# Kernel tuning notes

Hardware: AMD Instinct MI355X
Metric: run time of the kernel (lower is better)

Reference implementation:

```python
import jax, jax.numpy as jnp
import numpy as np
from jax import lax

HID, PROJ, DYN = 256, 256, 64
HW, BS, NQ = 6400, 16, 100


def setup_inputs() -> dict:
    key = jax.random.key(0)
    ks = jax.random.split(key, 10)
    p = lambda k, shape: jax.random.normal(k, shape, jnp.float32) * 0.02
    return {
        "query_feat": jax.random.normal(ks[0], (HW, BS, HID), jnp.float32),
        "support_feat": jax.random.normal(ks[1], (NQ, BS, HID), jnp.float32),
        "h": 80,
        "w": 80,
        "Wq": p(ks[2], (HID, PROJ)), "bq": jnp.zeros((PROJ,), jnp.float32),
        "Ws": p(ks[3], (HID, PROJ)), "bsp": jnp.zeros((PROJ,), jnp.float32),
        "W1": p(ks[4], (PROJ, DYN)), "b1": jnp.zeros((DYN,), jnp.float32),
        "W2": p(ks[5], (DYN, HID)), "b2": jnp.zeros((HID,), jnp.float32),
    }


def reference(query_feat, support_feat, h, w, Wq, bq, Ws, bsp, W1, b1, W2, b2):
    # query_feat: [hw, bs, c] -> [bs, hw, c]; support_feat: [nq, bs, c] -> [bs, nq, c]
    qf = jnp.transpose(query_feat, (1, 0, 2))
    sf = jnp.transpose(support_feat, (1, 0, 2))
    bsz, nq = sf.shape[0], sf.shape[1]
    hw = h * w

    fs_proj = sf @ Ws + bsp                      # [bs, nq, proj]
    fq_proj = qf @ Wq + bq                       # [bs, hw, proj]
    pattern = jnp.tanh(jax.nn.relu(fs_proj @ W1 + b1) @ W2 + b2)
    fs_feat = (pattern + 1.0) * fs_proj          # [bs, nq, proj]

    # bmm(fq, fs^T).T -> [bs, nq, hw]
    sim = jnp.einsum("bkp,bnp->bnk", fq_proj, fs_feat)
    similarity = sim.reshape(bsz, nq, h, w)

    # coordinate grid: x varies along w, y along h; flattened [hw, 2]
    gy = jnp.arange(h, dtype=jnp.float32) + 0.5
    gx = jnp.arange(w, dtype=jnp.float32) + 0.5
    X, Y = jnp.meshgrid(gx, gy, indexing="xy")  # each [h, w]
    coord = jnp.stack([X, Y], axis=-1).reshape(hw, 2)
    side = jnp.array([w, h], dtype=jnp.float32)

    sm = jax.nn.softmax(sim, axis=-1)            # [bs, nq, hw]
    proposal_for_loss = jnp.einsum("bnk,kd->bnd", sm, coord) / side

    # argmax peak -> one-hot -> 3x3 max-pool dilation (note (w,h) reshape per original)
    max_pos = jnp.argmax(sim, axis=-1)           # [bs, nq]
    max_mask = jax.nn.one_hot(max_pos, hw, dtype=jnp.float32).reshape(bsz, nq, w, h)
    local_mask = lax.reduce_window(
        max_mask, -jnp.inf, lax.max,
        window_dimensions=(1, 1, 3, 3), window_strides=(1, 1, 1, 1),
        padding=[(0, 0), (0, 0), (1, 1), (1, 1)],
    ).reshape(bsz, nq, hw)

    local_sm = sm * local_mask
    local_sm = local_sm / (jnp.sum(local_sm, axis=-1, keepdims=True) + 1e-10)
    proposals = jnp.einsum("bnk,kd->bnd", local_sm, coord) / side

    return proposal_for_loss, similarity, proposals
```

## Files before the change

### kernel.cpp

```cpp
#include <hip/hip_runtime.h>

#define HID 256
#define PROJ 256
#define DYN 64
#define HWD 6400
#define BSZ 16
#define NQ 100
#define HH 80
#define WW 80

typedef unsigned short u16;
typedef u16 u16x8 __attribute__((ext_vector_type(8)));
typedef __bf16 bf16x8 __attribute__((ext_vector_type(8)));
typedef float f32x4 __attribute__((ext_vector_type(4)));

__device__ __forceinline__ float bf2f(u16 h) {
    union { unsigned u; float f; } c; c.u = ((unsigned)h) << 16; return c.f;
}
__device__ __forceinline__ u16 f2bf(float f) {
    union { float f; unsigned u; } c; c.f = f;
    return (u16)((c.u + 0x7FFFu + ((c.u >> 16) & 1u)) >> 16);
}

__global__ __launch_bounds__(1024, 1) void kpre(
    const float* __restrict__ support,
    const float* __restrict__ Wq, const float* __restrict__ bq,
    const float* __restrict__ Ws, const float* __restrict__ bsp,
    const float* __restrict__ W1, const float* __restrict__ b1,
    const float* __restrict__ W2, const float* __restrict__ b2,
    u16* __restrict__ pack, float* __restrict__ cvec)
{
    const int c = blockIdx.x;
    const int b = blockIdx.y;
    const int t = threadIdx.x;

    __shared__ __align__(16) float sf_t[HID][8];
    __shared__ __align__(16) float part[4][8][256];
    __shared__ __align__(16) float fsp[8][PROJ];
    __shared__ __align__(16) float hidp[2][8][DYN];
    __shared__ __align__(16) float hid[8][DYN];
    __shared__ __align__(16) float fsf_t[PROJ][8];
    __shared__ float cacc[8][4];

    const int g = t >> 8;
    const int p = t & 255;

    {
        const int nl = t >> 7;
        const int i0 = (t & 127) * 2;
        const int n = c * 8 + nl;
        float v0 = 0.f, v1 = 0.f;
        if (n < NQ) {
            const float* sp = support + (size_t)n * (BSZ * HID) + (size_t)b * HID + i0;
            const float2 a = *reinterpret_cast<const float2*>(sp);
            v0 = a.x; v1 = a.y;
        }
        sf_t[i0][nl] = v0;
        sf_t[i0 + 1][nl] = v1;
    }
    __syncthreads();

    {
        float acc[8];
        #pragma unroll
        for (int n = 0; n < 8; ++n) acc[n] = 0.f;
        const int ibase = g * 64;
        #pragma unroll
        for (int ib = 0; ib < 64; ib += 32) {
            float w[32];
            #pragma unroll
            for (int j = 0; j < 32; ++j)
                w[j] = Ws[(size_t)(ibase + ib + j) * PROJ + p];
            #pragma unroll
            for (int j = 0; j < 32; ++j) {
                const f32x4 s0 = *reinterpret_cast<const f32x4*>(&sf_t[ibase + ib + j][0]);
                const f32x4 s1 = *reinterpret_cast<const f32x4*>(&sf_t[ibase + ib + j][4]);
                acc[0] += s0[0] * w[j]; acc[1] += s0[1] * w[j];
                acc[2] += s0[2] * w[j]; acc[3] += s0[3] * w[j];
                acc[4] += s1[0] * w[j]; acc[5] += s1[1] * w[j];
                acc[6] += s1[2] * w[j]; acc[7] += s1[3] * w[j];
            }
        }
        #pragma unroll
        for (int n = 0; n < 8; ++n) part[g][n][p] = acc[n];
    }
    __syncthreads();
    {
        const int na = t >> 8;
        const float bb = bsp[p];
        #pragma unroll
        for (int k = 0; k < 2; ++k) {
            const int n = na + k * 4;
            fsp[n][p] = part[0][n][p] + part[1][n][p] + part[2][n][p] + part[3][n][p] + bb;
        }
    }
    __syncthreads();

    {
        const int ph = t >> 9;
        const int n = (t >> 6) & 7;
        const int d = t & 63;
        float a = 0.f;
        const int pb0 = ph * 128;
        #pragma unroll
        for (int pb = 0; pb < 128; pb += 32) {
            float w[32];
            #pragma unroll
            for (int j = 0; j < 32; ++j)
                w[j] = W1[(size_t)(pb0 + pb + j) * DYN + d];
            #pragma unroll
            for (int j = 0; j < 32; j += 4) {
                const f32x4 s = *reinterpret_cast<const f32x4*>(&fsp[n][pb0 + pb + j]);
                a += s[0] * w[j] + s[1] * w[j + 1] + s[2] * w[j + 2] + s[3] * w[j + 3];
            }
        }
        hidp[ph][n][d] = a;
    }
    __syncthreads();
    if (t < 512) {
        const int n = t >> 6, d = t & 63;
        const float a = hidp[0][n][d] + hidp[1][n][d] + b1[d];
        hid[n][d] = a > 0.f ? a : 0.f;
    }
    __syncthreads();

    {
        const int nh = t >> 8;
        const int n0 = nh * 2, n1 = nh * 2 + 1;
        const float bqv = bq[p];
        const float b2v = b2[p];
        float w[64];
        #pragma unroll
        for (int d = 0; d < 64; ++d) w[d] = W2[(size_t)d * PROJ + p];
        float a0 = 0.f, a1 = 0.f;
        #pragma unroll
        for (int d0 = 0; d0 < 64; d0 += 4) {
            const f32x4 h0 = *reinterpret_cast<const f32x4*>(&hid[n0][d0]);
            const f32x4 h1 = *reinterpret_cast<const f32x4*>(&hid[n1][d0]);
            a0 += h0[0] * w[d0] + h0[1] * w[d0 + 1] + h0[2] * w[d0 + 2] + h0[3] * w[d0 + 3];
            a1 += h1[0] * w[d0] + h1[1] * w[d0 + 1] + h1[2] * w[d0 + 2] + h1[3] * w[d0 + 3];
        }
        const float pat0 = tanhf(a0 + b2v);
        const float pat1 = tanhf(a1 + b2v);
        const float ff0 = (pat0 + 1.f) * fsp[n0][p];
        const float ff1 = (pat1 + 1.f) * fsp[n1][p];
        *reinterpret_cast<float2*>(&fsf_t[p][n0]) = make_float2(ff0, ff1);
        float cp0 = bqv * ff0, cp1 = bqv * ff1;
        for (int off = 32; off > 0; off >>= 1) {
            cp0 += __shfl_down(cp0, off);
            cp1 += __shfl_down(cp1, off);
        }
        const int lane = t & 63;
        const int ps = (t >> 6) & 3;
        if (lane == 0) { cacc[n0][ps] = cp0; cacc[n1][ps] = cp1; }
    }
    __syncthreads();
    if (t < 8) {
        const int n = c * 8 + t;
        if (n < NQ) cvec[b * NQ + n] = cacc[t][0] + cacc[t][1] + cacc[t][2] + cacc[t][3];
    }

    {
        const int h = p;
        float acc[8];
        #pragma unroll
        for (int n = 0; n < 8; ++n) acc[n] = 0.f;
        const int pbase = g * 64;
        #pragma unroll
        for (int pb = 0; pb < 64; pb += 32) {
            f32x4 wv4[8];
            #pragma unroll
            for (int k = 0; k < 8; ++k)
                wv4[k] = *reinterpret_cast<const f32x4*>(Wq + (size_t)h * PROJ + pbase + pb + k * 4);
            #pragma unroll
            for (int k = 0; k < 8; ++k) {
                #pragma unroll
                for (int m = 0; m < 4; ++m) {
                    const int pp = pbase + pb + k * 4 + m;
                    const float w = wv4[k][m];
                    const f32x4 f0 = *reinterpret_cast<const f32x4*>(&fsf_t[pp][0]);
                    const f32x4 f1 = *reinterpret_cast<const f32x4*>(&fsf_t[pp][4]);
                    acc[0] += f0[0] * w; acc[1] += f0[1] * w;
                    acc[2] += f0[2] * w; acc[3] += f0[3] * w;
                    acc[4] += f1[0] * w; acc[5] += f1[1] * w;
                    acc[6] += f1[2] * w; acc[7] += f1[3] * w;
                }
            }
        }
        #pragma unroll
        for (int n = 0; n < 8; ++n) part[g][n][h] = acc[n];
    }
    __syncthreads();

    {
        const int h = p;
        const int na = t >> 8;
        const int ks = h >> 5, quad = (h >> 3) & 3, j = h & 7;
        const int nt = c >> 1;
        #pragma unroll
        for (int k = 0; k < 2; ++k) {
            const int nl = na + k * 4;
            const int n = c * 8 + nl;
            float f = part[0][nl][h] + part[1][nl][h] + part[2][nl][h] + part[3][nl][h];
            if (n >= NQ) f = 0.f;
            const u16 hi = f2bf(f);
            const u16 lo = f2bf(f - bf2f(hi));
            const int nit = (c & 1) * 8 + nl;
            const int lane2 = quad * 16 + nit;
            const size_t base = ((((size_t)b * 2 + 0) * 8 + ks) * 8 + nt) * 512 + lane2 * 8 + j;
            pack[base] = hi;
            pack[base + (size_t)8 * 8 * 512] = lo;
        }
    }
}

__global__ __launch_bounds__(256, 4) void ksim(
    const float* __restrict__ qf,
    const u16* __restrict__ pack,
    const float* __restrict__ cvec,
    float* __restrict__ sim)
{
    const int mc = blockIdx.x;
    const int b  = blockIdx.y;
    const int wv = threadIdx.x >> 6;
    const int lane = threadIdx.x & 63;
    const int quad = lane >> 4, l16 = lane & 15;

    f32x4 acc[7];
    #pragma unroll
    for (int nt = 0; nt < 7; ++nt) acc[nt] = (f32x4){0.f, 0.f, 0.f, 0.f};

    const int row = mc * 64 + wv * 16 + l16;
    const float* ap = qf + (size_t)row * (BSZ * HID) + b * HID + quad * 8;
    const u16* pb = pack + (size_t)b * (2 * 8 * 8 * 64 * 8) + (size_t)lane * 8;

    f32x4 a0 = *reinterpret_cast<const f32x4*>(ap + 0);
    f32x4 a1 = *reinterpret_cast<const f32x4*>(ap + 4);

    #pragma unroll
    for (int ks = 0; ks < 8; ++ks) {
        u16x8 uh[7], ul[7];
        #pragma unroll
        for (int nt = 0; nt < 7; ++nt) {
            uh[nt] = *reinterpret_cast<const u16x8*>(pb + ((size_t)(0 * 8 + ks) * 8 + nt) * 512);
            ul[nt] = *reinterpret_cast<const u16x8*>(pb + ((size_t)(1 * 8 + ks) * 8 + nt) * 512);
        }
        f32x4 n0, n1;
        if (ks < 7) {
            n0 = *reinterpret_cast<const f32x4*>(ap + (ks + 1) * 32 + 0);
            n1 = *reinterpret_cast<const f32x4*>(ap + (ks + 1) * 32 + 4);
        }
        bf16x8 ahi, alo;
        #pragma unroll
        for (int j = 0; j < 4; ++j) {
            const float v = a0[j];
            const __bf16 h = (__bf16)v;
            ahi[j] = h; alo[j] = (__bf16)(v - (float)h);
        }
        #pragma unroll
        for (int j = 0; j < 4; ++j) {
            const float v = a1[j];
            const __bf16 h = (__bf16)v;
            ahi[4 + j] = h; alo[4 + j] = (__bf16)(v - (float)h);
        }
        #pragma unroll
        for (int nt = 0; nt < 7; ++nt) {
            const bf16x8 bh = __builtin_bit_cast(bf16x8, uh[nt]);
            const bf16x8 bl = __builtin_bit_cast(bf16x8, ul[nt]);
            acc[nt] = __builtin_amdgcn_mfma_f32_16x16x32_bf16(ahi, bh, acc[nt], 0, 0, 0);
            acc[nt] = __builtin_amdgcn_mfma_f32_16x16x32_bf16(ahi, bl, acc[nt], 0, 0, 0);
            acc[nt] = __builtin_amdgcn_mfma_f32_16x16x32_bf16(alo, bh, acc[nt], 0, 0, 0);
        }
        a0 = n0; a1 = n1;
    }

    const int kbase = mc * 64 + wv * 16 + quad * 4;
    #pragma unroll
    for (int nt = 0; nt < 7; ++nt) {
        const int n = nt * 16 + l16;
        if (n >= NQ) continue;
        const float cadd = cvec[b * NQ + n];
        f32x4 o = acc[nt];
        o[0] += cadd; o[1] += cadd; o[2] += cadd; o[3] += cadd;
        *reinterpret_cast<f32x4*>(sim + (size_t)(b * NQ + n) * HWD + kbase) = o;
    }
}

__global__ __launch_bounds__(64, 4) void kfin(
    const float* __restrict__ sim,
    float* __restrict__ out)
{
    const int bn = blockIdx.x;
    const int lane = threadIdx.x;
    const float* src = sim + (size_t)bn * HWD;

    f32x4 v[25];
    #pragma unroll
    for (int j = 0; j < 25; ++j)
        v[j] = *reinterpret_cast<const f32x4*>(src + j * 256 + lane * 4);

    float bv = -3.4e38f; int bi = 0;
    #pragma unroll
    for (int j = 0; j < 25; ++j) {
        #pragma unroll
        for (int k = 0; k < 4; ++k) {
            if (v[j][k] > bv) { bv = v[j][k]; bi = j * 256 + lane * 4 + k; }
        }
    }
    #pragma unroll
    for (int m = 1; m < 64; m <<= 1) {
        const float ov = __shfl_xor(bv, m);
        const int oi = __shfl_xor(bi, m);
        if (ov > bv || (ov == bv && oi < bi)) { bv = ov; bi = oi; }
    }
    const int xc = bi % WW, yc = bi / WW;

    float s1 = 0.f, sx = 0.f, sy = 0.f;
    float wl = 0.f, wx = 0.f, wyv = 0.f;
    int x = (lane * 4) % WW, y = (lane * 4) / WW;
    #pragma unroll
    for (int j = 0; j < 25; ++j) {
        #pragma unroll
        for (int k = 0; k < 4; ++k) {
            int xe = x + k, ye = y;
            if (xe >= WW) { xe -= WW; ye += 1; }
            const float e = __expf(v[j][k] - bv);
            const float fx = (float)xe + 0.5f;
            const float fy = (float)ye + 0.5f;
            s1 += e; sx += e * fx; sy += e * fy;
            const int dx = xe - xc, dy = ye - yc;
            const bool inw = (dx >= -1 && dx <= 1 && dy >= -1 && dy <= 1);
            const float ew = inw ? e : 0.f;
            wl += ew; wx += ew * fx; wyv += ew * fy;
        }
        x += 16; y += 3;
        if (x >= WW) { x -= WW; y += 1; }
    }
    #pragma unroll
    for (int m = 1; m < 64; m <<= 1) {
        s1 += __shfl_xor(s1, m);
        sx += __shfl_xor(sx, m);
        sy += __shfl_xor(sy, m);
        wl += __shfl_xor(wl, m);
        wx += __shfl_xor(wx, m);
        wyv += __shfl_xor(wyv, m);
    }

    if (lane == 0) {
        const float invS = 1.f / s1;
        out[(size_t)bn * 2 + 0] = sx * invS / (float)WW;
        out[(size_t)bn * 2 + 1] = sy * invS / (float)HH;
        const float den = wl + 1e-10f * s1;
        const size_t pbase = 3200 + (size_t)BSZ * NQ * HWD;
        out[pbase + (size_t)bn * 2 + 0] = wx / den / (float)WW;
        out[pbase + (size_t)bn * 2 + 1] = wyv / den / (float)HH;
    }
}

extern "C" void kernel_launch(void* const* d_in, const int* in_sizes, int n_in,
                              void* d_out, int out_size, void* d_ws, size_t ws_size,
                              hipStream_t stream) {
    const float* qf  = (const float*)d_in[0];
    const float* sf  = (const float*)d_in[1];
    const float* Wq  = (const float*)d_in[4];
    const float* bq  = (const float*)d_in[5];
    const float* Ws  = (const float*)d_in[6];
    const float* bsp = (const float*)d_in[7];
    const float* W1  = (const float*)d_in[8];
    const float* b1  = (const float*)d_in[9];
    const float* W2  = (const float*)d_in[10];
    const float* b2  = (const float*)d_in[11];

    u16*   pack  = (u16*)d_ws;
    float* cvec  = (float*)((char*)d_ws + 2097152);
    float* out   = (float*)d_out;
    float* sim   = out + 3200;

    kpre<<<dim3(14, 16), 1024, 0, stream>>>(sf, Wq, bq, Ws, bsp, W1, b1, W2, b2, pack, cvec);
    ksim<<<dim3(100, 16), 256, 0, stream>>>(qf, pack, cvec, sim);
    kfin<<<1600, 64, 0, stream>>>(sim, out);
}
```

Measured before the change: 271.6 us.

## Split kfin rows across two waves and batch weight loads with sched barriers

The final softmax/argmax kernel now uses two waves per row, each handling about half of the 6400 elements. Partial argmax and weighted sums are combined through shared memory. In kpre, weight loads are batched into larger register arrays, and sched_barrier keeps all loads issued before the FMAs, which raises memory-level parallelism; ksim gets a similar barrier. This costs more registers and an extra block-level sync in kfin.

```diff
diff --git a/kernel.cpp b/kernel.cpp
--- a/kernel.cpp
+++ b/kernel.cpp
@@ -65,21 +65,19 @@
         #pragma unroll
         for (int n = 0; n < 8; ++n) acc[n] = 0.f;
         const int ibase = g * 64;
-        #pragma unroll
-        for (int ib = 0; ib < 64; ib += 32) {
-            float w[32];
-            #pragma unroll
-            for (int j = 0; j < 32; ++j)
-                w[j] = Ws[(size_t)(ibase + ib + j) * PROJ + p];
-            #pragma unroll
-            for (int j = 0; j < 32; ++j) {
-                const f32x4 s0 = *reinterpret_cast<const f32x4*>(&sf_t[ibase + ib + j][0]);
-                const f32x4 s1 = *reinterpret_cast<const f32x4*>(&sf_t[ibase + ib + j][4]);
-                acc[0] += s0[0] * w[j]; acc[1] += s0[1] * w[j];
-                acc[2] += s0[2] * w[j]; acc[3] += s0[3] * w[j];
-                acc[4] += s1[0] * w[j]; acc[5] += s1[1] * w[j];
-                acc[6] += s1[2] * w[j]; acc[7] += s1[3] * w[j];
-            }
+        float w[64];
+        #pragma unroll
+        for (int j = 0; j < 64; ++j)
+            w[j] = Ws[(size_t)(ibase + j) * PROJ + p];
+        __builtin_amdgcn_sched_barrier(0);
+        #pragma unroll
+        for (int j = 0; j < 64; ++j) {
+            const f32x4 s0 = *reinterpret_cast<const f32x4*>(&sf_t[ibase + j][0]);
+            const f32x4 s1 = *reinterpret_cast<const f32x4*>(&sf_t[ibase + j][4]);
+            acc[0] += s0[0] * w[j]; acc[1] += s0[1] * w[j];
+            acc[2] += s0[2] * w[j]; acc[3] += s0[3] * w[j];
+            acc[4] += s1[0] * w[j]; acc[5] += s1[1] * w[j];
+            acc[6] += s1[2] * w[j]; acc[7] += s1[3] * w[j];
         }
         #pragma unroll
         for (int n = 0; n < 8; ++n) part[g][n][p] = acc[n];
@@ -103,13 +101,14 @@
         float a = 0.f;
         const int pb0 = ph * 128;
         #pragma unroll
-        for (int pb = 0; pb < 128; pb += 32) {
-            float w[32];
+        for (int pb = 0; pb < 128; pb += 64) {
+            float w[64];
             #pragma unroll
-            for (int j = 0; j < 32; ++j)
+            for (int j = 0; j < 64; ++j)
                 w[j] = W1[(size_t)(pb0 + pb + j) * DYN + d];
+            __builtin_amdgcn_sched_barrier(0);
             #pragma unroll
-            for (int j = 0; j < 32; j += 4) {
+            for (int j = 0; j < 64; j += 4) {
                 const f32x4 s = *reinterpret_cast<const f32x4*>(&fsp[n][pb0 + pb + j]);
                 a += s[0] * w[j] + s[1] * w[j + 1] + s[2] * w[j + 2] + s[3] * w[j + 3];
             }
@@ -132,6 +131,7 @@
         float w[64];
         #pragma unroll
         for (int d = 0; d < 64; ++d) w[d] = W2[(size_t)d * PROJ + p];
+        __builtin_amdgcn_sched_barrier(0);
         float a0 = 0.f, a1 = 0.f;
         #pragma unroll
         for (int d0 = 0; d0 < 64; d0 += 4) {
@@ -166,25 +166,23 @@
         #pragma unroll
         for (int n = 0; n < 8; ++n) acc[n] = 0.f;
         const int pbase = g * 64;
-        #pragma unroll
-        for (int pb = 0; pb < 64; pb += 32) {
-            f32x4 wv4[8];
+        f32x4 wv4[16];
+        #pragma unroll
+        for (int k = 0; k < 16; ++k)
+            wv4[k] = *reinterpret_cast<const f32x4*>(Wq + (size_t)h * PROJ + pbase + k * 4);
+        __builtin_amdgcn_sched_barrier(0);
+        #pragma unroll
+        for (int k = 0; k < 16; ++k) {
             #pragma unroll
-            for (int k = 0; k < 8; ++k)
-                wv4[k] = *reinterpret_cast<const f32x4*>(Wq + (size_t)h * PROJ + pbase + pb + k * 4);
-            #pragma unroll
-            for (int k = 0; k < 8; ++k) {
-                #pragma unroll
-                for (int m = 0; m < 4; ++m) {
-                    const int pp = pbase + pb + k * 4 + m;
-                    const float w = wv4[k][m];
-                    const f32x4 f0 = *reinterpret_cast<const f32x4*>(&fsf_t[pp][0]);
-                    const f32x4 f1 = *reinterpret_cast<const f32x4*>(&fsf_t[pp][4]);
-                    acc[0] += f0[0] * w; acc[1] += f0[1] * w;
-                    acc[2] += f0[2] * w; acc[3] += f0[3] * w;
-                    acc[4] += f1[0] * w; acc[5] += f1[1] * w;
-                    acc[6] += f1[2] * w; acc[7] += f1[3] * w;
-                }
+            for (int m = 0; m < 4; ++m) {
+                const int pp = pbase + k * 4 + m;
+                const float w = wv4[k][m];
+                const f32x4 f0 = *reinterpret_cast<const f32x4*>(&fsf_t[pp][0]);
+                const f32x4 f1 = *reinterpret_cast<const f32x4*>(&fsf_t[pp][4]);
+                acc[0] += f0[0] * w; acc[1] += f0[1] * w;
+                acc[2] += f0[2] * w; acc[3] += f0[3] * w;
+                acc[4] += f1[0] * w; acc[5] += f1[1] * w;
+                acc[6] += f1[2] * w; acc[7] += f1[3] * w;
             }
         }
         #pragma unroll
@@ -250,6 +248,7 @@
             n0 = *reinterpret_cast<const f32x4*>(ap + (ks + 1) * 32 + 0);
             n1 = *reinterpret_cast<const f32x4*>(ap + (ks + 1) * 32 + 4);
         }
+        __builtin_amdgcn_sched_barrier(0);
         bf16x8 ahi, alo;
         #pragma unroll
         for (int j = 0; j < 4; ++j) {
@@ -286,25 +285,35 @@
     }
 }
 
-__global__ __launch_bounds__(64, 4) void kfin(
+__global__ __launch_bounds__(128, 2) void kfin(
     const float* __restrict__ sim,
     float* __restrict__ out)
 {
     const int bn = blockIdx.x;
-    const int lane = threadIdx.x;
+    const int w = threadIdx.x >> 6;
+    const int lane = threadIdx.x & 63;
     const float* src = sim + (size_t)bn * HWD;
 
-    f32x4 v[25];
-    #pragma unroll
-    for (int j = 0; j < 25; ++j)
-        v[j] = *reinterpret_cast<const f32x4*>(src + j * 256 + lane * 4);
-
-    float bv = -3.4e38f; int bi = 0;
-    #pragma unroll
-    for (int j = 0; j < 25; ++j) {
-        #pragma unroll
-        for (int k = 0; k < 4; ++k) {
-            if (v[j][k] > bv) { bv = v[j][k]; bi = j * 256 + lane * 4 + k; }
+    __shared__ float redf[2][8];
+
+    const int base = w ? 12 : 0;
+    const int cnt  = w ? 13 : 12;
+
+    f32x4 v[13];
+    #pragma unroll
+    for (int j = 0; j < 13; ++j)
+        if (j < cnt)
+            v[j] = *reinterpret_cast<const f32x4*>(src + (base + j) * 256 + lane * 4);
+    __builtin_amdgcn_sched_barrier(0);
+
+    float bv = -3.4e38f; int bi = 0x7FFFFFFF;
+    #pragma unroll
+    for (int j = 0; j < 13; ++j) {
+        if (j < cnt) {
+            #pragma unroll
+            for (int k = 0; k < 4; ++k) {
+                if (v[j][k] > bv) { bv = v[j][k]; bi = (base + j) * 256 + lane * 4 + k; }
+            }
         }
     }
     #pragma unroll
@@ -313,25 +322,36 @@
         const int oi = __shfl_xor(bi, m);
         if (ov > bv || (ov == bv && oi < bi)) { bv = ov; bi = oi; }
     }
+    if (lane == 0) { redf[w][0] = bv; redf[w][1] = __int_as_float(bi); }
+    __syncthreads();
+    {
+        const float v0 = redf[0][0], v1 = redf[1][0];
+        const int i0 = __float_as_int(redf[0][1]), i1 = __float_as_int(redf[1][1]);
+        if (v1 > v0 || (v1 == v0 && i1 < i0)) { bv = v1; bi = i1; }
+        else { bv = v0; bi = i0; }
+    }
     const int xc = bi % WW, yc = bi / WW;
 
     float s1 = 0.f, sx = 0.f, sy = 0.f;
     float wl = 0.f, wx = 0.f, wyv = 0.f;
-    int x = (lane * 4) % WW, y = (lane * 4) / WW;
-    #pragma unroll
-    for (int j = 0; j < 25; ++j) {
-        #pragma unroll
-        for (int k = 0; k < 4; ++k) {
-            int xe = x + k, ye = y;
-            if (xe >= WW) { xe -= WW; ye += 1; }
-            const float e = __expf(v[j][k] - bv);
-            const float fx = (float)xe + 0.5f;
-            const float fy = (float)ye + 0.5f;
-            s1 += e; sx += e * fx; sy += e * fy;
-            const int dx = xe - xc, dy = ye - yc;
-            const bool inw = (dx >= -1 && dx <= 1 && dy >= -1 && dy <= 1);
-            const float ew = inw ? e : 0.f;
-            wl += ew; wx += ew * fx; wyv += ew * fy;
+    const int g0 = base * 256 + lane * 4;
+    int x = g0 % WW, y = g0 / WW;
+    #pragma unroll
+    for (int j = 0; j < 13; ++j) {
+        if (j < cnt) {
+            #pragma unroll
+            for (int k = 0; k < 4; ++k) {
+                int xe = x + k, ye = y;
+                if (xe >= WW) { xe -= WW; ye += 1; }
+                const float e = __expf(v[j][k] - bv);
+                const float fx = (float)xe + 0.5f;
+                const float fy = (float)ye + 0.5f;
+                s1 += e; sx += e * fx; sy += e * fy;
+                const int dx = xe - xc, dy = ye - yc;
+                const bool inw = (dx >= -1 && dx <= 1 && dy >= -1 && dy <= 1);
+                const float ew = inw ? e : 0.f;
+                wl += ew; wx += ew * fx; wyv += ew * fy;
+            }
         }
         x += 16; y += 3;
         if (x >= WW) { x -= WW; y += 1; }
@@ -345,15 +365,26 @@
         wx += __shfl_xor(wx, m);
         wyv += __shfl_xor(wyv, m);
     }
-
     if (lane == 0) {
-        const float invS = 1.f / s1;
-        out[(size_t)bn * 2 + 0] = sx * invS / (float)WW;
-        out[(size_t)bn * 2 + 1] = sy * invS / (float)HH;
-        const float den = wl + 1e-10f * s1;
+        redf[w][2] = s1; redf[w][3] = sx; redf[w][4] = sy;
+        redf[w][5] = wl; redf[w][6] = wx; redf[w][7] = wyv;
+    }
+    __syncthreads();
+
+    if (w == 0 && lane == 0) {
+        const float S1 = redf[0][2] + redf[1][2];
+        const float SX = redf[0][3] + redf[1][3];
+        const float SY = redf[0][4] + redf[1][4];
+        const float WL = redf[0][5] + redf[1][5];
+        const float WX = redf[0][6] + redf[1][6];
+        const float WY = redf[0][7] + redf[1][7];
+        const float invS = 1.f / S1;
+        out[(size_t)bn * 2 + 0] = SX * invS / (float)WW;
+        out[(size_t)bn * 2 + 1] = SY * invS / (float)HH;
+        const float den = WL + 1e-10f * S1;
         const size_t pbase = 3200 + (size_t)BSZ * NQ * HWD;
-        out[pbase + (size_t)bn * 2 + 0] = wx / den / (float)WW;
-        out[pbase + (size_t)bn * 2 + 1] = wyv / den / (float)HH;
+        out[pbase + (size_t)bn * 2 + 0] = WX / den / (float)WW;
+        out[pbase + (size_t)bn * 2 + 1] = WY / den / (float)HH;
     }
 }
 
@@ -378,5 +409,5 @@
 
     kpre<<<dim3(14, 16), 1024, 0, stream>>>(sf, Wq, bq, Ws, bsp, W1, b1, W2, b2, pack, cvec);
     ksim<<<dim3(100, 16), 256, 0, stream>>>(qf, pack, cvec, sim);
-    kfin<<<1600, 64, 0, stream>>>(sim, out);
-}
+    kfin<<<1600, 64 * 2, 0, stream>>>(sim, out);
+}
```

Result: faster. 262.3 us (-3.4%).
